# Optimization experiments

Hardware: AMD Instinct MI355X
Metric: run time of the kernel (lower is better)

## Reference

```python
import jax, jax.numpy as jnp
import numpy as np

NUM_HEADS = 8
B, S, D = 4, 2048, 512


def setup_inputs() -> dict:
    key = jax.random.key(0)
    ks = jax.random.split(key, 12)
    scale = 1.0 / np.sqrt(D)
    return {
        "v": jax.random.normal(ks[0], (B, S, D), dtype=jnp.float32),
        "k": jax.random.normal(ks[1], (B, S, D), dtype=jnp.float32),
        "q": jax.random.normal(ks[2], (B, S, D), dtype=jnp.float32),
        "Wq": jax.random.normal(ks[3], (D, D), dtype=jnp.float32) * scale,
        "bq": jnp.zeros((D,), dtype=jnp.float32),
        "Wk": jax.random.normal(ks[4], (D, D), dtype=jnp.float32) * scale,
        "bk": jnp.zeros((D,), dtype=jnp.float32),
        "Wv": jax.random.normal(ks[5], (D, D), dtype=jnp.float32) * scale,
        "bv": jnp.zeros((D,), dtype=jnp.float32),
        "Wo": jax.random.normal(ks[6], (D, D), dtype=jnp.float32) * scale,
        "bo": jnp.zeros((D,), dtype=jnp.float32),
        "top_k": 32,
    }


def reference(v, k, q, Wq, bq, Wk, bk, Wv, bv, Wo, bo, top_k):
    dh = D // NUM_HEADS  # per-head depth

    def split_heads(x):  # [B,S,D] -> [B,H,S,dh]
        return x.reshape(B, -1, NUM_HEADS, dh).transpose(0, 2, 1, 3)

    qh = split_heads(q @ Wq + bq)
    kh = split_heads(k @ Wk + bk)
    vh = split_heads(v @ Wv + bv)

    logits = jnp.einsum('bhqd,bhkd->bhqk', qh, kh) / jnp.sqrt(jnp.float32(dh))
    w = jax.nn.softmax(logits, axis=-1)  # [B,H,S,S]

    num_keys = w.shape[-1]
    if top_k < num_keys:
        vals, idx = jax.lax.top_k(w, top_k)  # [B,H,S,top_k]
        bb = jnp.arange(B)[:, None, None, None]
        hh = jnp.arange(NUM_HEADS)[None, :, None, None]
        qq = jnp.arange(S)[None, None, :, None]
        sparse = jnp.zeros_like(w).at[bb, hh, qq, idx].set(vals)
        # tf.linalg.normalize(ord=1): divide by L1 norm along last axis
        w = sparse / jnp.sum(jnp.abs(sparse), axis=-1, keepdims=True)

    attn = jnp.einsum('bhqk,bhkd->bhqd', w, vh)  # [B,H,S,dh]
    concat = attn.transpose(0, 2, 1, 3).reshape(B, -1, D)
    out = concat @ Wo + bo
    return (out, w)
```

## Files before the change

### kernel.cpp

```cpp
#include <hip/hip_runtime.h>
#include <hip/hip_bf16.h>
#include <stdint.h>

#define S_LEN 2048
#define DMODEL 512
#define NH 8
#define DH 64
#define TOPK 32
#define CMAX 128
#define LO_SCALE 4096.0f
#define INV_LO (1.0f/4096.0f)

typedef _Float16 f16;
typedef f16 half8 __attribute__((ext_vector_type(8)));
typedef f16 half4 __attribute__((ext_vector_type(4)));
typedef float floatx4 __attribute__((ext_vector_type(4)));
typedef float f32x4 __attribute__((ext_vector_type(4)));

#define AS1 __attribute__((address_space(1)))
#define AS3 __attribute__((address_space(3)))

__device__ __forceinline__ void gl_lds16(const void* g, void* l) {
    __builtin_amdgcn_global_load_lds((const AS1 void*)g, (AS3 void*)l, 16, 0, 0);
}

__global__ __launch_bounds__(256)
void gemm_proj(const float* __restrict__ X, const float* __restrict__ W,
               const float* __restrict__ bias, float* __restrict__ out, int mode)
{
    __shared__ float As[16][132];
    __shared__ float Bs[16][132];
    const int tid = threadIdx.x;
    const int tx = tid & 15;
    const int ty = tid >> 4;
    const int m0 = blockIdx.y * 128;
    const int n0 = blockIdx.x * 128;

    float acc[8][8];
#pragma unroll
    for (int i = 0; i < 8; ++i)
#pragma unroll
        for (int j = 0; j < 8; ++j) acc[i][j] = 0.f;

    for (int k0 = 0; k0 < 512; k0 += 16) {
#pragma unroll
        for (int u = 0; u < 2; ++u) {
            int id = tid + u * 256;
            int r  = id >> 2;
            int c4 = (id & 3) * 4;
            float4 a = *(const float4*)(X + (size_t)(m0 + r) * 512 + k0 + c4);
            As[c4 + 0][r] = a.x; As[c4 + 1][r] = a.y;
            As[c4 + 2][r] = a.z; As[c4 + 3][r] = a.w;
            int rb = id >> 5;
            int cb = (id & 31) * 4;
            *(float4*)&Bs[rb][cb] = *(const float4*)(W + (size_t)(k0 + rb) * 512 + n0 + cb);
        }
        __syncthreads();
#pragma unroll
        for (int kk = 0; kk < 16; ++kk) {
            float a[8], b[8];
            *(float4*)&a[0] = *(const float4*)&As[kk][ty * 8];
            *(float4*)&a[4] = *(const float4*)&As[kk][ty * 8 + 4];
            *(float4*)&b[0] = *(const float4*)&Bs[kk][tx * 8];
            *(float4*)&b[4] = *(const float4*)&Bs[kk][tx * 8 + 4];
#pragma unroll
            for (int i = 0; i < 8; ++i)
#pragma unroll
                for (int j = 0; j < 8; ++j)
                    acc[i][j] = fmaf(a[i], b[j], acc[i][j]);
        }
        __syncthreads();
    }

    float bb[8];
    *(float4*)&bb[0] = *(const float4*)(bias + n0 + tx * 8);
    *(float4*)&bb[4] = *(const float4*)(bias + n0 + tx * 8 + 4);

    const int c = n0 + tx * 8;
#pragma unroll
    for (int i = 0; i < 8; ++i) {
        int r = m0 + ty * 8 + i;
        float4 w0 = make_float4(acc[i][0] + bb[0], acc[i][1] + bb[1],
                                acc[i][2] + bb[2], acc[i][3] + bb[3]);
        float4 w1 = make_float4(acc[i][4] + bb[4], acc[i][5] + bb[5],
                                acc[i][6] + bb[6], acc[i][7] + bb[7]);
        if (mode == 0) {
            int b_ = r >> 11, s = r & 2047, h = c >> 6, d = c & 63;
            float* p = out + (((size_t)(b_ * NH + h) * S_LEN) + s) * DH + d;
            *(float4*)p = w0; *(float4*)(p + 4) = w1;
        } else {
            float* p = out + (size_t)r * 512 + c;
            *(float4*)p = w0; *(float4*)(p + 4) = w1;
        }
    }
}

__global__ __launch_bounds__(256)
void gemm_logits(const float* __restrict__ Qh, const float* __restrict__ Kh,
                 float* __restrict__ logits)
{
    __shared__ float As[32][132];
    __shared__ float Bs[32][132];
    const int tid = threadIdx.x;
    const int tx = tid & 15;
    const int ty = tid >> 4;
    const int bh = blockIdx.z;
    const float* Ab = Qh + (size_t)bh * S_LEN * DH;
    const float* Bb = Kh + (size_t)bh * S_LEN * DH;
    const int q0 = blockIdx.y * 128;
    const int k0 = blockIdx.x * 128;

    float acc[8][8];
#pragma unroll
    for (int i = 0; i < 8; ++i)
#pragma unroll
        for (int j = 0; j < 8; ++j) acc[i][j] = 0.f;

    for (int kh = 0; kh < 64; kh += 32) {
#pragma unroll
        for (int u = 0; u < 4; ++u) {
            int id = tid + u * 256;
            int r  = id >> 3;
            int c4 = (id & 7) * 4;
            float4 a = *(const float4*)(Ab + (size_t)(q0 + r) * DH + kh + c4);
            As[c4 + 0][r] = a.x * 0.125f; As[c4 + 1][r] = a.y * 0.125f;
            As[c4 + 2][r] = a.z * 0.125f; As[c4 + 3][r] = a.w * 0.125f;
            float4 b = *(const float4*)(Bb + (size_t)(k0 + r) * DH + kh + c4);
            Bs[c4 + 0][r] = b.x; Bs[c4 + 1][r] = b.y;
            Bs[c4 + 2][r] = b.z; Bs[c4 + 3][r] = b.w;
        }
        __syncthreads();
#pragma unroll
        for (int kk = 0; kk < 32; ++kk) {
            float a[8], b[8];
            *(float4*)&a[0] = *(const float4*)&As[kk][ty * 8];
            *(float4*)&a[4] = *(const float4*)&As[kk][ty * 8 + 4];
            *(float4*)&b[0] = *(const float4*)&Bs[kk][tx * 8];
            *(float4*)&b[4] = *(const float4*)&Bs[kk][tx * 8 + 4];
#pragma unroll
            for (int i = 0; i < 8; ++i)
#pragma unroll
                for (int j = 0; j < 8; ++j)
                    acc[i][j] = fmaf(a[i], b[j], acc[i][j]);
        }
        __syncthreads();
    }

    float* C = logits + (size_t)bh * S_LEN * S_LEN + (size_t)(q0 + ty * 8) * S_LEN + k0 + tx * 8;
#pragma unroll
    for (int i = 0; i < 8; ++i) {
        *(float4*)(C + (size_t)i * S_LEN)     = make_float4(acc[i][0], acc[i][1], acc[i][2], acc[i][3]);
        *(float4*)(C + (size_t)i * S_LEN + 4) = make_float4(acc[i][4], acc[i][5], acc[i][6], acc[i][7]);
    }
}

__global__ __launch_bounds__(256)
void wsplit2(const float* __restrict__ W0, const float* __restrict__ W1,
             f16* __restrict__ planes)
{
    __shared__ float tile[32][33];
    const float* W = blockIdx.z ? W1 : W0;
    f16* Th = planes + (size_t)blockIdx.z * 524288;
    f16* Tl = Th + 262144;
    const int bx = blockIdx.x * 32;
    const int by = blockIdx.y * 32;
    const int lx = threadIdx.x & 31, ly = threadIdx.x >> 5;
#pragma unroll
    for (int r = ly; r < 32; r += 8)
        tile[r][lx] = W[(size_t)(by + r) * 512 + bx + lx];
    __syncthreads();
#pragma unroll
    for (int r = ly; r < 32; r += 8) {
        float x = tile[lx][r];
        f16 h = (f16)x;
        f16 l = (f16)((x - (float)h) * LO_SCALE);
        Th[(size_t)(bx + r) * 512 + by + lx] = h;
        Tl[(size_t)(bx + r) * 512 + by + lx] = l;
    }
}

__global__ __launch_bounds__(256)
void gemm_x32(const float* __restrict__ X,
              const f16* __restrict__ Bh_, const f16* __restrict__ Bl_,
              const float* __restrict__ bias, float* __restrict__ outF, int mode)
{
    __shared__ f16 sm[16384];
    f16* As_h = sm;       f16* As_l = sm + 4096;
    f16* Bs_h = sm + 8192; f16* Bs_l = sm + 12288;
    const int tid  = threadIdx.x;
    const int lane = tid & 63, wv = tid >> 6;
    const int wm = wv & 1, wn = wv >> 1;
    const int quad = lane >> 4, l15 = lane & 15;
    const int m0 = blockIdx.y * 128, n0 = blockIdx.x * 128;

    floatx4 acc_h[4][4], acc_c[4][4];
    const floatx4 z4 = {0.f, 0.f, 0.f, 0.f};
#pragma unroll
    for (int i = 0; i < 4; ++i)
#pragma unroll
        for (int j = 0; j < 4; ++j) { acc_h[i][j] = z4; acc_c[i][j] = z4; }

    for (int k0 = 0; k0 < 512; k0 += 32) {
        __syncthreads();
#pragma unroll
        for (int c = 0; c < 4; ++c) {
            int r   = c * 32 + (tid >> 3);
            int col = (tid & 7) * 4;
            float4 x = *(const float4*)(X + (size_t)(m0 + r) * 512 + k0 + col);
            f16 h0 = (f16)x.x, h1 = (f16)x.y, h2 = (f16)x.z, h3 = (f16)x.w;
            half4 hv = {h0, h1, h2, h3};
            half4 lv = {(f16)((x.x - (float)h0) * LO_SCALE),
                        (f16)((x.y - (float)h1) * LO_SCALE),
                        (f16)((x.z - (float)h2) * LO_SCALE),
                        (f16)((x.w - (float)h3) * LO_SCALE)};
            *(half4*)&As_h[r * 32 + col] = hv;
            *(half4*)&As_l[r * 32 + col] = lv;
        }
#pragma unroll
        for (int c = 0; c < 2; ++c) {
            int r    = c * 64 + (wv << 4) + (lane >> 2);
            int ch   = (lane & 3) * 8;
            int lidx = (c * 64 + (wv << 4)) * 32 + lane * 8;
            gl_lds16(Bh_ + (size_t)(n0 + r) * 512 + k0 + ch, &Bs_h[lidx]);
            gl_lds16(Bl_ + (size_t)(n0 + r) * 512 + k0 + ch, &Bs_l[lidx]);
        }
        asm volatile("s_waitcnt vmcnt(0)" ::: "memory");
        __syncthreads();

        half8 bh8[4], bl8[4];
#pragma unroll
        for (int j = 0; j < 4; ++j) {
            int n = wn * 64 + j * 16 + l15;
            bh8[j] = *(const half8*)&Bs_h[n * 32 + quad * 8];
            bl8[j] = *(const half8*)&Bs_l[n * 32 + quad * 8];
        }
#pragma unroll
        for (int i = 0; i < 4; ++i) {
            int m = wm * 64 + i * 16 + l15;
            half8 ah = *(const half8*)&As_h[m * 32 + quad * 8];
            half8 al = *(const half8*)&As_l[m * 32 + quad * 8];
#pragma unroll
            for (int j = 0; j < 4; ++j) {
                acc_h[i][j] = __builtin_amdgcn_mfma_f32_16x16x32_f16(ah, bh8[j], acc_h[i][j], 0, 0, 0);
                acc_c[i][j] = __builtin_amdgcn_mfma_f32_16x16x32_f16(ah, bl8[j], acc_c[i][j], 0, 0, 0);
                acc_c[i][j] = __builtin_amdgcn_mfma_f32_16x16x32_f16(al, bh8[j], acc_c[i][j], 0, 0, 0);
            }
        }
    }

#pragma unroll
    for (int j = 0; j < 4; ++j) {
        int col = n0 + wn * 64 + j * 16 + l15;
        float bv = bias[col];
#pragma unroll
        for (int i = 0; i < 4; ++i) {
            int rbase = m0 + wm * 64 + i * 16 + quad * 4;
#pragma unroll
            for (int rg = 0; rg < 4; ++rg) {
                float r = acc_h[i][j][rg] + acc_c[i][j][rg] * INV_LO + bv;
                int row = rbase + rg;
                if (mode == 2) {
                    outF[(size_t)row * 512 + col] = r;
                } else {
                    int b_ = row >> 11, s = row & 2047, h = col >> 6, d = col & 63;
                    outF[(((size_t)(b_ * NH + h)) * S_LEN + s) * DH + d] = r;
                }
            }
        }
    }
}

__global__ __launch_bounds__(256)
void gemm_x16(const f16* __restrict__ Ah_, const f16* __restrict__ Al_,
              const f16* __restrict__ Bh_, const f16* __restrict__ Bl_,
              const float* __restrict__ bias, float* __restrict__ outF,
              int Ksz, int ldc, int mode)
{
    __shared__ f16 sm[16384];
    f16* As_h = sm;        f16* As_l = sm + 4096;
    f16* Bs_h = sm + 8192; f16* Bs_l = sm + 12288;
    const int tid  = threadIdx.x;
    const int lane = tid & 63, wv = tid >> 6;
    const int wm = wv & 1, wn = wv >> 1;
    const int quad = lane >> 4, l15 = lane & 15;
    const int m0 = blockIdx.y * 128, n0 = blockIdx.x * 128;

    floatx4 acc_h[4][4], acc_c[4][4];
    const floatx4 z4 = {0.f, 0.f, 0.f, 0.f};
#pragma unroll
    for (int i = 0; i < 4; ++i)
#pragma unroll
        for (int j = 0; j < 4; ++j) { acc_h[i][j] = z4; acc_c[i][j] = z4; }

    for (int k0 = 0; k0 < Ksz; k0 += 32) {
        __syncthreads();
#pragma unroll
        for (int c = 0; c < 2; ++c) {
            int r    = c * 64 + (wv << 4) + (lane >> 2);
            int ch   = (lane & 3) * 8;
            int lidx = (c * 64 + (wv << 4)) * 32 + lane * 8;
            gl_lds16(Ah_ + (size_t)(m0 + r) * Ksz + k0 + ch, &As_h[lidx]);
            gl_lds16(Al_ + (size_t)(m0 + r) * Ksz + k0 + ch, &As_l[lidx]);
            gl_lds16(Bh_ + (size_t)(n0 + r) * Ksz + k0 + ch, &Bs_h[lidx]);
            gl_lds16(Bl_ + (size_t)(n0 + r) * Ksz + k0 + ch, &Bs_l[lidx]);
        }
        asm volatile("s_waitcnt vmcnt(0)" ::: "memory");
        __syncthreads();

        half8 bh8[4], bl8[4];
#pragma unroll
        for (int j = 0; j < 4; ++j) {
            int n = wn * 64 + j * 16 + l15;
            bh8[j] = *(const half8*)&Bs_h[n * 32 + quad * 8];
            bl8[j] = *(const half8*)&Bs_l[n * 32 + quad * 8];
        }
#pragma unroll
        for (int i = 0; i < 4; ++i) {
            int m = wm * 64 + i * 16 + l15;
            half8 ah = *(const half8*)&As_h[m * 32 + quad * 8];
            half8 al = *(const half8*)&As_l[m * 32 + quad * 8];
#pragma unroll
            for (int j = 0; j < 4; ++j) {
                acc_h[i][j] = __builtin_amdgcn_mfma_f32_16x16x32_f16(ah, bh8[j], acc_h[i][j], 0, 0, 0);
                acc_c[i][j] = __builtin_amdgcn_mfma_f32_16x16x32_f16(ah, bl8[j], acc_c[i][j], 0, 0, 0);
                acc_c[i][j] = __builtin_amdgcn_mfma_f32_16x16x32_f16(al, bh8[j], acc_c[i][j], 0, 0, 0);
            }
        }
    }

#pragma unroll
    for (int j = 0; j < 4; ++j) {
        int col = n0 + wn * 64 + j * 16 + l15;
        float bv = (mode == 2) ? bias[col] : 0.f;
#pragma unroll
        for (int i = 0; i < 4; ++i) {
            int rbase = m0 + wm * 64 + i * 16 + quad * 4;
#pragma unroll
            for (int rg = 0; rg < 4; ++rg) {
                float r = acc_h[i][j][rg] + acc_c[i][j][rg] * INV_LO;
                int row = rbase + rg;
                outF[(size_t)row * ldc + col] = r + bv;
            }
        }
    }
}

__device__ __forceinline__ unsigned sortable_u(float f) {
    unsigned u = __float_as_uint(f);
    return u ^ ((unsigned)(((int)u) >> 31) | 0x80000000u);
}

__global__ __launch_bounds__(256)
void topk_attn(float* __restrict__ wbuf, const float* __restrict__ Vh,
               f16* __restrict__ attH, f16* __restrict__ attL)
{
    __shared__ float    wrow[4][2048];
    __shared__ uint64_t cand[4][CMAX];
    __shared__ float    win_w[4][TOPK];
    __shared__ int      win_i[4][TOPK];

    const int tid  = threadIdx.x;
    const int wv   = tid >> 6;
    const int lane = tid & 63;
    const unsigned long long lt = (1ull << lane) - 1ull;
    const int row = blockIdx.x * 4 + wv;
    float* wr = wbuf + (size_t)row * 2048;

    if (lane < TOPK) { win_w[wv][lane] = 0.f; win_i[wv][lane] = 0; }

    float L[32];
#pragma unroll
    for (int t = 0; t < 8; ++t) {
        f32x4 x = *(const f32x4*)(wr + t * 256 + lane * 4);
        L[4 * t + 0] = x.x; L[4 * t + 1] = x.y; L[4 * t + 2] = x.z; L[4 * t + 3] = x.w;
    }

    float m = L[0];
#pragma unroll
    for (int t = 1; t < 32; ++t) m = fmaxf(m, L[t]);
#pragma unroll
    for (int off = 32; off > 0; off >>= 1) m = fmaxf(m, __shfl_xor(m, off, 64));

    auto wcount = [&](float T) -> int {
        int c = 0;
#pragma unroll
        for (int t = 0; t < 32; ++t) c += (int)__popcll(__ballot(L[t] >= T));
        return c;
    };

    float delta = 2.f;
    int clo = wcount(m - delta);
    int guard = 0;
    while (clo < TOPK && guard < 8) { delta *= 16.f; clo = wcount(m - delta); ++guard; }
    float Tlo = m - delta, Thi = m;
    guard = 0;
    while (clo > 64 && guard < 40) {
        float mid = 0.5f * (Tlo + Thi);
        int cc = wcount(mid);
        if (cc >= TOPK) { Tlo = mid; clo = cc; } else { Thi = mid; }
        ++guard;
    }
    const int nc = min(clo, CMAX);

    int base = 0;
#pragma unroll
    for (int t = 0; t < 32; ++t) {
        bool p = (L[t] >= Tlo);
        unsigned long long mk = __ballot(p);
        if (p) {
            int pos = base + (int)__popcll(mk & lt);
            if (pos < CMAX) {
                int idx = (t >> 2) * 256 + (lane << 2) + (t & 3);
                cand[wv][pos] = ((uint64_t)sortable_u(L[t]) << 32) | (uint32_t)(~(uint32_t)idx);
            }
        }
        base += (int)__popcll(mk);
    }
    __syncthreads();

    float mysum = 0.f;
    int wbase = 0;
    const int passes = (nc + 63) >> 6;
    for (int it = 0; it < passes; ++it) {
        int ci = (it << 6) + lane;
        bool have = ci < nc;
        uint64_t mykey = have ? cand[wv][ci] : 0ull;
        int rank = 0;
#pragma unroll 8
        for (int j = 0; j < nc; ++j)
            rank += (cand[wv][j] > mykey) ? 1 : 0;
        bool win = have && (rank < TOPK);
        unsigned long long mk = __ballot(win);
        if (win) {
            int pos = wbase + (int)__popcll(mk & lt);
            unsigned uv = (unsigned)(mykey >> 32);
            unsigned fu = (uv & 0x80000000u) ? (uv ^ 0x80000000u) : ~uv;
            float v = __uint_as_float(fu);
            int idx = (int)(~(uint32_t)mykey);
            float e = __expf(v - m);
            win_w[wv][pos] = e;
            win_i[wv][pos] = idx;
            mysum += e;
        }
        wbase += (int)__popcll(mk);
    }
#pragma unroll
    for (int off = 32; off > 0; off >>= 1) mysum += __shfl_xor(mysum, off, 64);
    const float rw = 1.f / mysum;
    __syncthreads();

    const f32x4 z = {0.f, 0.f, 0.f, 0.f};
#pragma unroll
    for (int t = 0; t < 8; ++t) ((f32x4*)wrow[wv])[t * 64 + lane] = z;
    __syncthreads();
    if (lane < TOPK) wrow[wv][win_i[wv][lane] & 2047] = win_w[wv][lane] * rw;
    __syncthreads();
#pragma unroll
    for (int t = 0; t < 8; ++t)
        __builtin_nontemporal_store(((f32x4*)wrow[wv])[t * 64 + lane],
                                    (f32x4*)(wr + (size_t)(t * 64 + lane) * 4));

    const int bh = row >> 11;
    const float* Vb = Vh + (size_t)bh * S_LEN * DH;
    float acc = 0.f;
#pragma unroll
    for (int j = 0; j < TOPK; ++j) {
        float wj = win_w[wv][j] * rw;
        int   kj = win_i[wv][j];
        acc = fmaf(wj, Vb[(size_t)kj * DH + lane], acc);
    }
    const int b_ = row >> 14;
    const int h  = (row >> 11) & 7;
    const int s  = row & 2047;
    size_t oidx = (((size_t)b_ * S_LEN) + s) * 512 + h * DH + lane;
    f16 hh = (f16)acc;
    attH[oidx] = hh;
    attL[oidx] = (f16)((acc - (float)hh) * LO_SCALE);
}

extern "C" void kernel_launch(void* const* d_in, const int* in_sizes, int n_in,
                              void* d_out, int out_size, void* d_ws, size_t ws_size,
                              hipStream_t stream) {
    const float* v  = (const float*)d_in[0];
    const float* k  = (const float*)d_in[1];
    const float* q  = (const float*)d_in[2];
    const float* Wq = (const float*)d_in[3];
    const float* bq = (const float*)d_in[4];
    const float* Wk = (const float*)d_in[5];
    const float* bk = (const float*)d_in[6];
    const float* Wv = (const float*)d_in[7];
    const float* bv = (const float*)d_in[8];
    const float* Wo = (const float*)d_in[9];
    const float* bo = (const float*)d_in[10];

    float* out  = (float*)d_out;
    float* wout = out + (size_t)4 * S_LEN * 512;

    char* ws = (char*)d_ws;
    float* Vh   = (float*)ws;
    float* Qh32 = (float*)(ws + 16777216);
    float* Kh32 = (float*)(ws + 33554432);
    f16* WT  = (f16*)(ws + 50331648);
    f16 *WvH = WT,           *WvL = WT + 262144;
    f16 *WoH = WT + 524288,  *WoL = WT + 786432;
    f16* attH = (f16*)(ws + 16777216);
    f16* attL = (f16*)(ws + 25165824);

    wsplit2<<<dim3(16, 16, 2), 256, 0, stream>>>(Wv, Wo, WT);

    dim3 gP(4, 64);
    gemm_proj<<<gP, 256, 0, stream>>>(q, Wq, bq, Qh32, 0);
    gemm_proj<<<gP, 256, 0, stream>>>(k, Wk, bk, Kh32, 0);
    gemm_x32<<<gP, 256, 0, stream>>>(v, WvH, WvL, bv, Vh, 1);

    gemm_logits<<<dim3(16, 16, 32), 256, 0, stream>>>(Qh32, Kh32, wout);

    topk_attn<<<16384, 256, 0, stream>>>(wout, Vh, attH, attL);

    gemm_x16<<<dim3(4, 64, 1), 256, 0, stream>>>(attH, attL, WoH, WoL, bo, out, 512, 512, 2);
}
```

Baseline: 1.299 ms.

## Merge Q/K projections, prefetch GEMM tiles, use nontemporal stores, relax topk barriers

Q and K projections now run in one launch, with the z grid dimension selecting the operand set. That kernel uses a 32-wide k tile and register prefetch of the next tile during compute, and the logits GEMM gets the same prefetch. Logits are written and read with nontemporal hints, since the 512MB matrix cannot stay in cache. In topk_attn, the per-wave LDS zeroing moves earlier and block-wide __syncthreads are replaced with per-wave lgkmcnt waits, which is valid only because each wave touches only its own LDS rows. Larger tiles raise LDS use and register pressure.

```diff
diff --git a/kernel.cpp b/kernel.cpp
--- a/kernel.cpp
+++ b/kernel.cpp
@@ -23,13 +23,22 @@
 __device__ __forceinline__ void gl_lds16(const void* g, void* l) {
     __builtin_amdgcn_global_load_lds((const AS1 void*)g, (AS3 void*)l, 16, 0, 0);
 }
+__device__ __forceinline__ void lds_fence() {
+    asm volatile("s_waitcnt lgkmcnt(0)" ::: "memory");
+}
 
 __global__ __launch_bounds__(256)
-void gemm_proj(const float* __restrict__ X, const float* __restrict__ W,
-               const float* __restrict__ bias, float* __restrict__ out, int mode)
+void qkproj(const float* __restrict__ Xq, const float* __restrict__ Xk,
+            const float* __restrict__ Wq_, const float* __restrict__ Wk_,
+            const float* __restrict__ bq_, const float* __restrict__ bk_,
+            float* __restrict__ outQ, float* __restrict__ outK)
 {
-    __shared__ float As[16][132];
-    __shared__ float Bs[16][132];
+    __shared__ float As[32][132];
+    __shared__ float Bs[32][132];
+    const float* X    = blockIdx.z ? Xk  : Xq;
+    const float* W    = blockIdx.z ? Wk_ : Wq_;
+    const float* bias = blockIdx.z ? bk_ : bq_;
+    float* out        = blockIdx.z ? outK : outQ;
     const int tid = threadIdx.x;
     const int tx = tid & 15;
     const int ty = tid >> 4;
@@ -42,27 +51,41 @@
 #pragma unroll
         for (int j = 0; j < 8; ++j) acc[i][j] = 0.f;
 
-    for (int k0 = 0; k0 < 512; k0 += 16) {
-#pragma unroll
-        for (int u = 0; u < 2; ++u) {
+    f32x4 pa[4], pb[4];
+#pragma unroll
+    for (int u = 0; u < 4; ++u) {
+        int id = tid + u * 256;
+        pa[u] = *(const f32x4*)(X + (size_t)(m0 + (id >> 3)) * 512 + (id & 7) * 4);
+        pb[u] = *(const f32x4*)(W + (size_t)(id >> 5) * 512 + n0 + (id & 31) * 4);
+    }
+
+    for (int k0 = 0; k0 < 512; k0 += 32) {
+#pragma unroll
+        for (int u = 0; u < 4; ++u) {
             int id = tid + u * 256;
-            int r  = id >> 2;
-            int c4 = (id & 3) * 4;
-            float4 a = *(const float4*)(X + (size_t)(m0 + r) * 512 + k0 + c4);
-            As[c4 + 0][r] = a.x; As[c4 + 1][r] = a.y;
-            As[c4 + 2][r] = a.z; As[c4 + 3][r] = a.w;
-            int rb = id >> 5;
-            int cb = (id & 31) * 4;
-            *(float4*)&Bs[rb][cb] = *(const float4*)(W + (size_t)(k0 + rb) * 512 + n0 + cb);
-        }
-        __syncthreads();
-#pragma unroll
-        for (int kk = 0; kk < 16; ++kk) {
+            int r = id >> 3, c4 = (id & 7) * 4;
+            As[c4 + 0][r] = pa[u].x; As[c4 + 1][r] = pa[u].y;
+            As[c4 + 2][r] = pa[u].z; As[c4 + 3][r] = pa[u].w;
+            int rb = id >> 5, cb = (id & 31) * 4;
+            *(f32x4*)&Bs[rb][cb] = pb[u];
+        }
+        __syncthreads();
+        if (k0 < 480) {
+            int kn = k0 + 32;
+#pragma unroll
+            for (int u = 0; u < 4; ++u) {
+                int id = tid + u * 256;
+                pa[u] = *(const f32x4*)(X + (size_t)(m0 + (id >> 3)) * 512 + kn + (id & 7) * 4);
+                pb[u] = *(const f32x4*)(W + (size_t)(kn + (id >> 5)) * 512 + n0 + (id & 31) * 4);
+            }
+        }
+#pragma unroll
+        for (int kk = 0; kk < 32; ++kk) {
             float a[8], b[8];
-            *(float4*)&a[0] = *(const float4*)&As[kk][ty * 8];
-            *(float4*)&a[4] = *(const float4*)&As[kk][ty * 8 + 4];
-            *(float4*)&b[0] = *(const float4*)&Bs[kk][tx * 8];
-            *(float4*)&b[4] = *(const float4*)&Bs[kk][tx * 8 + 4];
+            *(f32x4*)&a[0] = *(const f32x4*)&As[kk][ty * 8];
+            *(f32x4*)&a[4] = *(const f32x4*)&As[kk][ty * 8 + 4];
+            *(f32x4*)&b[0] = *(const f32x4*)&Bs[kk][tx * 8];
+            *(f32x4*)&b[4] = *(const f32x4*)&Bs[kk][tx * 8 + 4];
 #pragma unroll
             for (int i = 0; i < 8; ++i)
 #pragma unroll
@@ -73,25 +96,18 @@
     }
 
     float bb[8];
-    *(float4*)&bb[0] = *(const float4*)(bias + n0 + tx * 8);
-    *(float4*)&bb[4] = *(const float4*)(bias + n0 + tx * 8 + 4);
+    *(f32x4*)&bb[0] = *(const f32x4*)(bias + n0 + tx * 8);
+    *(f32x4*)&bb[4] = *(const f32x4*)(bias + n0 + tx * 8 + 4);
 
     const int c = n0 + tx * 8;
 #pragma unroll
     for (int i = 0; i < 8; ++i) {
         int r = m0 + ty * 8 + i;
-        float4 w0 = make_float4(acc[i][0] + bb[0], acc[i][1] + bb[1],
-                                acc[i][2] + bb[2], acc[i][3] + bb[3]);
-        float4 w1 = make_float4(acc[i][4] + bb[4], acc[i][5] + bb[5],
-                                acc[i][6] + bb[6], acc[i][7] + bb[7]);
-        if (mode == 0) {
-            int b_ = r >> 11, s = r & 2047, h = c >> 6, d = c & 63;
-            float* p = out + (((size_t)(b_ * NH + h) * S_LEN) + s) * DH + d;
-            *(float4*)p = w0; *(float4*)(p + 4) = w1;
-        } else {
-            float* p = out + (size_t)r * 512 + c;
-            *(float4*)p = w0; *(float4*)(p + 4) = w1;
-        }
+        f32x4 w0 = {acc[i][0] + bb[0], acc[i][1] + bb[1], acc[i][2] + bb[2], acc[i][3] + bb[3]};
+        f32x4 w1 = {acc[i][4] + bb[4], acc[i][5] + bb[5], acc[i][6] + bb[6], acc[i][7] + bb[7]};
+        int b_ = r >> 11, s = r & 2047, h = c >> 6, d = c & 63;
+        float* p = out + (((size_t)(b_ * NH + h) * S_LEN) + s) * DH + d;
+        *(f32x4*)p = w0; *(f32x4*)(p + 4) = w1;
     }
 }
 
@@ -116,27 +132,42 @@
 #pragma unroll
         for (int j = 0; j < 8; ++j) acc[i][j] = 0.f;
 
-    for (int kh = 0; kh < 64; kh += 32) {
+    f32x4 qa[4], kb[4];
+#pragma unroll
+    for (int u = 0; u < 4; ++u) {
+        int id = tid + u * 256;
+        int r = id >> 3, c4 = (id & 7) * 4;
+        qa[u] = *(const f32x4*)(Ab + (size_t)(q0 + r) * DH + c4);
+        kb[u] = *(const f32x4*)(Bb + (size_t)(k0 + r) * DH + c4);
+    }
+
+    for (int ch = 0; ch < 2; ++ch) {
 #pragma unroll
         for (int u = 0; u < 4; ++u) {
             int id = tid + u * 256;
-            int r  = id >> 3;
-            int c4 = (id & 7) * 4;
-            float4 a = *(const float4*)(Ab + (size_t)(q0 + r) * DH + kh + c4);
-            As[c4 + 0][r] = a.x * 0.125f; As[c4 + 1][r] = a.y * 0.125f;
-            As[c4 + 2][r] = a.z * 0.125f; As[c4 + 3][r] = a.w * 0.125f;
-            float4 b = *(const float4*)(Bb + (size_t)(k0 + r) * DH + kh + c4);
-            Bs[c4 + 0][r] = b.x; Bs[c4 + 1][r] = b.y;
-            Bs[c4 + 2][r] = b.z; Bs[c4 + 3][r] = b.w;
-        }
-        __syncthreads();
+            int r = id >> 3, c4 = (id & 7) * 4;
+            As[c4 + 0][r] = qa[u].x * 0.125f; As[c4 + 1][r] = qa[u].y * 0.125f;
+            As[c4 + 2][r] = qa[u].z * 0.125f; As[c4 + 3][r] = qa[u].w * 0.125f;
+            Bs[c4 + 0][r] = kb[u].x; Bs[c4 + 1][r] = kb[u].y;
+            Bs[c4 + 2][r] = kb[u].z; Bs[c4 + 3][r] = kb[u].w;
+        }
+        __syncthreads();
+        if (ch == 0) {
+#pragma unroll
+            for (int u = 0; u < 4; ++u) {
+                int id = tid + u * 256;
+                int r = id >> 3, c4 = (id & 7) * 4;
+                qa[u] = *(const f32x4*)(Ab + (size_t)(q0 + r) * DH + 32 + c4);
+                kb[u] = *(const f32x4*)(Bb + (size_t)(k0 + r) * DH + 32 + c4);
+            }
+        }
 #pragma unroll
         for (int kk = 0; kk < 32; ++kk) {
             float a[8], b[8];
-            *(float4*)&a[0] = *(const float4*)&As[kk][ty * 8];
-            *(float4*)&a[4] = *(const float4*)&As[kk][ty * 8 + 4];
-            *(float4*)&b[0] = *(const float4*)&Bs[kk][tx * 8];
-            *(float4*)&b[4] = *(const float4*)&Bs[kk][tx * 8 + 4];
+            *(f32x4*)&a[0] = *(const f32x4*)&As[kk][ty * 8];
+            *(f32x4*)&a[4] = *(const f32x4*)&As[kk][ty * 8 + 4];
+            *(f32x4*)&b[0] = *(const f32x4*)&Bs[kk][tx * 8];
+            *(f32x4*)&b[4] = *(const f32x4*)&Bs[kk][tx * 8 + 4];
 #pragma unroll
             for (int i = 0; i < 8; ++i)
 #pragma unroll
@@ -149,8 +180,10 @@
     float* C = logits + (size_t)bh * S_LEN * S_LEN + (size_t)(q0 + ty * 8) * S_LEN + k0 + tx * 8;
 #pragma unroll
     for (int i = 0; i < 8; ++i) {
-        *(float4*)(C + (size_t)i * S_LEN)     = make_float4(acc[i][0], acc[i][1], acc[i][2], acc[i][3]);
-        *(float4*)(C + (size_t)i * S_LEN + 4) = make_float4(acc[i][4], acc[i][5], acc[i][6], acc[i][7]);
+        f32x4 v0 = {acc[i][0], acc[i][1], acc[i][2], acc[i][3]};
+        f32x4 v1 = {acc[i][4], acc[i][5], acc[i][6], acc[i][7]};
+        __builtin_nontemporal_store(v0, (f32x4*)(C + (size_t)i * S_LEN));
+        __builtin_nontemporal_store(v1, (f32x4*)(C + (size_t)i * S_LEN + 4));
     }
 }
 
@@ -206,7 +239,7 @@
         for (int c = 0; c < 4; ++c) {
             int r   = c * 32 + (tid >> 3);
             int col = (tid & 7) * 4;
-            float4 x = *(const float4*)(X + (size_t)(m0 + r) * 512 + k0 + col);
+            f32x4 x = *(const f32x4*)(X + (size_t)(m0 + r) * 512 + k0 + col);
             f16 h0 = (f16)x.x, h1 = (f16)x.y, h2 = (f16)x.z, h3 = (f16)x.w;
             half4 hv = {h0, h1, h2, h3};
             half4 lv = {(f16)((x.x - (float)h0) * LO_SCALE),
@@ -371,9 +404,13 @@
     float L[32];
 #pragma unroll
     for (int t = 0; t < 8; ++t) {
-        f32x4 x = *(const f32x4*)(wr + t * 256 + lane * 4);
+        f32x4 x = __builtin_nontemporal_load((const f32x4*)(wr + t * 256 + lane * 4));
         L[4 * t + 0] = x.x; L[4 * t + 1] = x.y; L[4 * t + 2] = x.z; L[4 * t + 3] = x.w;
     }
+
+    const f32x4 z = {0.f, 0.f, 0.f, 0.f};
+#pragma unroll
+    for (int t = 0; t < 8; ++t) ((f32x4*)wrow[wv])[t * 64 + lane] = z;
 
     float m = L[0];
 #pragma unroll
@@ -416,7 +453,7 @@
         }
         base += (int)__popcll(mk);
     }
-    __syncthreads();
+    lds_fence();
 
     float mysum = 0.f;
     int wbase = 0;
@@ -447,14 +484,11 @@
 #pragma unroll
     for (int off = 32; off > 0; off >>= 1) mysum += __shfl_xor(mysum, off, 64);
     const float rw = 1.f / mysum;
-    __syncthreads();
-
-    const f32x4 z = {0.f, 0.f, 0.f, 0.f};
-#pragma unroll
-    for (int t = 0; t < 8; ++t) ((f32x4*)wrow[wv])[t * 64 + lane] = z;
-    __syncthreads();
+    lds_fence();
+
     if (lane < TOPK) wrow[wv][win_i[wv][lane] & 2047] = win_w[wv][lane] * rw;
-    __syncthreads();
+    lds_fence();
+
 #pragma unroll
     for (int t = 0; t < 8; ++t)
         __builtin_nontemporal_store(((f32x4*)wrow[wv])[t * 64 + lane],
@@ -508,10 +542,8 @@
 
     wsplit2<<<dim3(16, 16, 2), 256, 0, stream>>>(Wv, Wo, WT);
 
-    dim3 gP(4, 64);
-    gemm_proj<<<gP, 256, 0, stream>>>(q, Wq, bq, Qh32, 0);
-    gemm_proj<<<gP, 256, 0, stream>>>(k, Wk, bk, Kh32, 0);
-    gemm_x32<<<gP, 256, 0, stream>>>(v, WvH, WvL, bv, Vh, 1);
+    qkproj<<<dim3(4, 64, 2), 256, 0, stream>>>(q, k, Wq, Wk, bq, bk, Qh32, Kh32);
+    gemm_x32<<<dim3(4, 64), 256, 0, stream>>>(v, WvH, WvL, bv, Vh, 1);
 
     gemm_logits<<<dim3(16, 16, 32), 256, 0, stream>>>(Qh32, Kh32, wout);
 
```

After: 1.121 ms. -13.7%, faster.
